# Kernel tuning notes

Hardware: AMD Instinct MI355X
Metric: run time of the kernel (lower is better)

Reference implementation:

```python
import jax, jax.numpy as jnp
import numpy as np

B, T, C = 2, 1024, 1024
HS = 64
H = C // HS                 # 16 wkv heads
C_ATT = 512
H_GQA = C_ATT // HS         # 8 kv heads
GROUP = H // H_GQA          # 2
D_DECAY, D_AAA, D_MV, D_GATE = 64, 64, 32, 160


def setup_inputs() -> dict:
    key = jax.random.key(0)
    ks = jax.random.split(key, 16)
    f32 = jnp.float32
    rn = lambda k, shp, s=0.02: jax.random.normal(k, shp, dtype=f32) * s
    return {
        'x': jax.random.normal(ks[0], (B, T, C), f32),
        'wkv_state_in': jnp.zeros((B, H, HS, HS), f32),
        'v_first_val': jax.random.normal(ks[1], (B, T, C), f32),
        'w0': jnp.linspace(-6.5, -1.5, C, dtype=f32).reshape(1, 1, C) + 0.5,
        'w1': rn(ks[2], (C, D_DECAY)), 'w2': rn(ks[3], (D_DECAY, C)),
        'a0': jnp.zeros((1, 1, C), f32),
        'a1': rn(ks[4], (C, D_AAA)), 'a2': rn(ks[5], (D_AAA, C)),
        'v0': jnp.ones((1, 1, C), f32),
        'v1': rn(ks[6], (C, D_MV)), 'v2': rn(ks[7], (D_MV, C)),
        'g1': rn(ks[8], (C, D_GATE)), 'g2': rn(ks[9], (D_GATE, C)),
        'k_k': jnp.full((1, 1, C), 0.85, f32),
        'k_a': jnp.ones((1, 1, C), f32),
        'r_k': rn(ks[10], (H, HS)),
        'Wq': rn(ks[11], (C, C)), 'Wk': rn(ks[12], (C_ATT, C)),
        'Wv': rn(ks[13], (C_ATT, C)), 'Wo': rn(ks[14], (C, C)),
        'ln_w': jnp.ones((C,), f32), 'ln_b': jnp.zeros((C,), f32),
    }


def _gqa_expand(t):
    # [B,T,C_ATT] -> repeat each kv head GROUP times -> [B,T,C]
    t = t.reshape(B, T, H_GQA, 1, HS)
    return jnp.broadcast_to(t, (B, T, H_GQA, GROUP, HS)).reshape(B, T, C)


def _wkv_scan(r, decay, k, v, a, b, S0):
    # all seq tensors [B,T,H,N]; scan over time with state S [B,H,N,N]
    seq = tuple(x.transpose(1, 0, 2, 3) for x in (r, decay, k, v, a, b))

    def step(S, ins):
        r_t, w_t, k_t, v_t, a_t, b_t = ins  # [B,H,N]
        sa = jnp.einsum('bhij,bhj->bhi', S, a_t)
        S = (S * w_t[:, :, None, :]
             + sa[..., None] * b_t[:, :, None, :]
             + v_t[..., None] * k_t[:, :, None, :])
        y = jnp.einsum('bhij,bhj->bhi', S, r_t)
        return S, y

    S_out, ys = jax.lax.scan(step, S0, seq)
    return ys.transpose(1, 0, 2, 3), S_out  # [B,T,H,N], [B,H,N,N]


def _forward(x, wkv_state_in, v_first_val, w0, w1, w2, a0, a1, a2, v0, v1, v2,
             g1, g2, k_k, k_a, r_k, Wq, Wk, Wv, Wo, ln_w, ln_b):
    r = x @ Wq.T                                   # [B,T,C]
    w = w0 + jnp.tanh(x @ w1) @ w2                 # decay logits [B,T,C]
    k = _gqa_expand(x @ Wk.T)                      # [B,T,C]
    v = _gqa_expand(x @ Wv.T)
    g = jax.nn.sigmoid(x @ g1) @ g2                # gate
    iclr = jax.nn.sigmoid(a0 + (x @ a1) @ a2)      # in-context learning rate

    kk = (k * k_k).reshape(B, T, H, HS)
    kk = kk / jnp.maximum(jnp.linalg.norm(kk, axis=-1, keepdims=True), 1e-12)
    kk = kk.reshape(B, T, C)

    iclr = 1.0 + (iclr - 1.0) * k_a
    k = k * iclr
    # layer_id > 0: mix v toward v_first
    v = v + (v_first_val - v) * jax.nn.sigmoid(v0 + (x @ v1) @ v2)

    decay = jnp.exp(-jnp.exp(w))                   # per-channel decay in (0,1)
    hv = lambda t: t.reshape(B, T, H, HS)
    xx, S_out = _wkv_scan(hv(r), hv(decay), hv(k), hv(v), hv(-kk), hv(kk * iclr), wkv_state_in)

    # GroupNorm with n_head groups, eps = 1e-5 * head_size
    mu = xx.mean(-1, keepdims=True)
    var = xx.var(-1, keepdims=True)
    xn = (xx - mu) * jax.lax.rsqrt(var + 1e-5 * HS)
    xn = xn.reshape(B, T, C) * ln_w + ln_b

    # r_k bonus term (standard RWKV7 epilogue)
    bonus = ((hv(r) * hv(k) * r_k).sum(-1, keepdims=True) * hv(v)).reshape(B, T, C)
    xn = xn + bonus

    out = (xn * g) @ Wo.T
    return out, S_out, v_first_val


def reference(x, wkv_state_in, v_first_val, w0, w1, w2, a0, a1, a2, v0, v1, v2,
              g1, g2, k_k, k_a, r_k, Wq, Wk, Wv, Wo, ln_w, ln_b):
    return _forward(x, wkv_state_in, v_first_val, w0, w1, w2, a0, a1, a2,
                    v0, v1, v2, g1, g2, k_k, k_a, r_k, Wq, Wk, Wv, Wo, ln_w, ln_b)
```

## Files before the change

### kernel.cpp

```cpp
#include <hip/hip_runtime.h>

typedef unsigned short u16;
typedef __attribute__((ext_vector_type(8))) short s16x8;
typedef __attribute__((ext_vector_type(4))) float f32x4;
typedef __attribute__((ext_vector_type(4))) int   i32x4;
typedef __attribute__((ext_vector_type(2))) int   i32x2;
typedef __attribute__((ext_vector_type(4))) unsigned short u16x4;

constexpr size_t OFF_XB   = 0;
constexpr size_t OFF_WQB  = OFF_XB   + 4194304;
constexpr size_t OFF_WKB  = OFF_WQB  + 2097152;
constexpr size_t OFF_WVB  = OFF_WKB  + 1048576;
constexpr size_t OFF_WOB  = OFF_WVB  + 1048576;
constexpr size_t OFF_W1T  = OFF_WOB  + 2097152;
constexpr size_t OFF_W2T  = OFF_W1T  + 786432;
constexpr size_t OFF_A2T  = OFF_W2T  + 131072;
constexpr size_t OFF_V2T  = OFF_A2T  + 131072;
constexpr size_t OFF_G2T  = OFF_V2T  + 65536;
constexpr size_t OFF_KQF  = OFF_G2T  + 327680;
constexpr size_t OFF_VQF  = OFF_KQF  + 4194304;
constexpr size_t OFF_URAW = OFF_VQF  + 4194304;
constexpr size_t OFF_UB   = OFF_URAW + 2621440;
constexpr size_t OFF_S2A  = OFF_UB   + 1572864;
constexpr size_t OFF_S2V  = OFF_S2A  + 8388608;
constexpr size_t OFF_GBUF = OFF_S2V  + 8388608;
constexpr size_t OFF_SEQ  = OFF_GBUF + 8388608;
constexpr size_t OFF_YBUF = OFF_SEQ  + 50331648;
constexpr size_t OFF_XGB  = OFF_YBUF + 8388608;

constexpr size_t OFF_VEPI = OFF_XB;
constexpr size_t OFF_DP   = OFF_W1T;

__device__ __forceinline__ u16 f2bf(float f){
  unsigned int u = __builtin_bit_cast(unsigned int, f);
  u = u + 0x7fffu + ((u >> 16) & 1u);
  return (u16)(u >> 16);
}
__device__ __forceinline__ int pk2(float a, float b){
  return (int)((unsigned)f2bf(a) | ((unsigned)f2bf(b) << 16));
}
__device__ __forceinline__ int cvtpk(float a, float b){
  int r;
  asm("v_cvt_pk_bf16_f32 %0, %1, %2" : "=v"(r) : "v"(a), "v"(b));
  return r;
}
__device__ __forceinline__ float bf2f(u16 h){
  return __builtin_bit_cast(float, ((unsigned)h) << 16);
}
__device__ __forceinline__ f32x4 cvt4(i32x2 v){
  unsigned a=(unsigned)v[0], b=(unsigned)v[1];
  f32x4 r;
  r[0]=__builtin_bit_cast(float, a<<16);
  r[1]=__builtin_bit_cast(float, a&0xffff0000u);
  r[2]=__builtin_bit_cast(float, b<<16);
  r[3]=__builtin_bit_cast(float, b&0xffff0000u);
  return r;
}

__device__ __forceinline__ void gload_lds16(const float* g, float* l){
  __builtin_amdgcn_global_load_lds((const __attribute__((address_space(1))) void*)g,
                                   (__attribute__((address_space(3))) void*)l, 16, 0, 0);
}
__device__ __forceinline__ void gload_lds16u(const u16* g, u16* l){
  __builtin_amdgcn_global_load_lds((const __attribute__((address_space(1))) void*)g,
                                   (__attribute__((address_space(3))) void*)l, 16, 0, 0);
}
__device__ __forceinline__ void gload_lds4(const float* g, float* l){
  __builtin_amdgcn_global_load_lds((const __attribute__((address_space(1))) void*)g,
                                   (__attribute__((address_space(3))) void*)l, 4, 0, 0);
}

constexpr size_t N_XB=2097152, N_WQ=1048576, N_WK=524288, N_WV=524288, N_WO=1048576,
  N_W1T=393216, N_W2T=65536, N_A2T=65536, N_V2T=32768, N_G2T=163840, N_VF=2097152;
constexpr size_t PREP_TOT = N_XB+N_WQ+N_WK+N_WV+N_WO+N_W1T+N_W2T+N_A2T+N_V2T+N_G2T+N_VF;

__global__ __launch_bounds__(256) void prep_kernel(char* ws, const float* x, const float* vfirst,
  const float* w1, const float* w2, const float* a1, const float* a2,
  const float* v1, const float* v2, const float* g1, const float* g2,
  const float* Wq, const float* Wk, const float* Wv, const float* Wo, float* dout)
{
  u16* XB=(u16*)(ws+OFF_XB); u16* WQB=(u16*)(ws+OFF_WQB); u16* WKB=(u16*)(ws+OFF_WKB);
  u16* WVB=(u16*)(ws+OFF_WVB); u16* WOB=(u16*)(ws+OFF_WOB); u16* W1T=(u16*)(ws+OFF_W1T);
  u16* W2T=(u16*)(ws+OFF_W2T); u16* A2T=(u16*)(ws+OFF_A2T); u16* V2T=(u16*)(ws+OFF_V2T);
  u16* G2T=(u16*)(ws+OFF_G2T);
  for (size_t idx=(size_t)blockIdx.x*256+threadIdx.x; idx<PREP_TOT; idx+=(size_t)gridDim.x*256){
    size_t r = idx;
    if (r < N_XB){ XB[r]=f2bf(x[r]); continue; } r-=N_XB;
    if (r < N_WQ){ WQB[r]=f2bf(Wq[r]); continue; } r-=N_WQ;
    if (r < N_WK){ WKB[r]=f2bf(Wk[r]); continue; } r-=N_WK;
    if (r < N_WV){ WVB[r]=f2bf(Wv[r]); continue; } r-=N_WV;
    if (r < N_WO){ WOB[r]=f2bf(Wo[r]); continue; } r-=N_WO;
    if (r < N_W1T){
      int n=(int)(r>>10), k=(int)(r&1023); float v=0.f;
      if (n<64) v=w1[(size_t)k*64+n];
      else if (n<128) v=a1[(size_t)k*64+(n-64)];
      else if (n<160) v=v1[(size_t)k*32+(n-128)];
      else if (n<320) v=g1[(size_t)k*160+(n-160)];
      W1T[r]=f2bf(v); continue; } r-=N_W1T;
    if (r < N_W2T){ int c=(int)(r>>6), d=(int)(r&63); W2T[r]=f2bf(w2[(size_t)d*1024+c]); continue; } r-=N_W2T;
    if (r < N_A2T){ int c=(int)(r>>6), d=(int)(r&63); A2T[r]=f2bf(a2[(size_t)d*1024+c]); continue; } r-=N_A2T;
    if (r < N_V2T){ int c=(int)(r>>5), d=(int)(r&31); V2T[r]=f2bf(v2[(size_t)d*1024+c]); continue; } r-=N_V2T;
    if (r < N_G2T){ int c=(int)(r/160), d=(int)(r%160); G2T[r]=f2bf(g2[(size_t)d*1024+c]); continue; } r-=N_G2T;
    dout[2228224 + r] = vfirst[r];
  }
}

__global__ __launch_bounds__(256) void gemm_kernel(int phase, char* ws,
  const float* w0b, const float* a0b, const float* v0b, float* dout)
{
  const u16* A; const u16* Bw;
  float* outF=nullptr; const float* bias=nullptr;
  char* SEQc=(char*)(ws+OFF_SEQ);
  u16* UBp=(u16*)(ws+OFF_UB);
  int lda=0, ldb=0, K=0, ldc=0, Nlim=1024, col0=0, outMode=0;
  int y = blockIdx.y;
  if (phase==0){
    A=(const u16*)(ws+OFF_XB); lda=1024; K=1024;
    if (y<8)      { Bw=(const u16*)(ws+OFF_WQB); ldb=1024; col0=y*128;       outMode=1; }
    else if (y<12){ Bw=(const u16*)(ws+OFF_WKB); ldb=1024; col0=(y-8)*128;   outF=(float*)(ws+OFF_KQF); ldc=512; Nlim=512; }
    else if (y<16){ Bw=(const u16*)(ws+OFF_WVB); ldb=1024; col0=(y-12)*128;  outF=(float*)(ws+OFF_VQF); ldc=512; Nlim=512; }
    else          { Bw=(const u16*)(ws+OFF_W1T); ldb=1024; col0=(y-16)*128;  outMode=4; Nlim=320; }
  } else if (phase==1){
    int seg=y>>3; col0=(y&7)*128;
    const int Ks[4]={64,64,32,160};
    const int Ao[4]={0,64,128,160};
    K=Ks[seg]; lda=384; ldb=K;
    A=(const u16*)(ws+OFF_UB) + Ao[seg];
    if (seg==0)     { Bw=(const u16*)(ws+OFF_W2T); outMode=2; bias=w0b; }
    else if (seg==1){ Bw=(const u16*)(ws+OFF_A2T); outMode=3; bias=a0b; outF=(float*)(ws+OFF_S2A); ldc=1024; }
    else if (seg==2){ Bw=(const u16*)(ws+OFF_V2T); outMode=3; bias=v0b; outF=(float*)(ws+OFF_S2V); ldc=1024; }
    else            { Bw=(const u16*)(ws+OFF_G2T); outF=(float*)(ws+OFF_GBUF); ldc=1024; }
  } else {
    A=(const u16*)(ws+OFF_XGB); lda=1024; K=1024;
    Bw=(const u16*)(ws+OFF_WOB); ldb=1024; col0=y*128; outF=dout; ldc=1024;
  }
  int m0 = blockIdx.x*128;
  __shared__ __align__(16) u16 As[2][4096];
  __shared__ __align__(16) u16 Bs[2][4096];
  int tid=threadIdx.x, l=tid&63, wv=tid>>6, wm=wv>>1, wn=wv&1;

  int srow = wv*32 + (l>>2);
  int cswz = (l&3) ^ ((srow>>1)&3);
  const u16* aP0 = A  + (size_t)(m0+srow)*lda      + cswz*8;
  const u16* aP1 = A  + (size_t)(m0+srow+16)*lda   + cswz*8;
  const u16* bP0 = Bw + (size_t)(col0+srow)*ldb    + cswz*8;
  const u16* bP1 = Bw + (size_t)(col0+srow+16)*ldb + cswz*8;

  f32x4 acc[4][4];
  #pragma unroll
  for (int i=0;i<4;i++)
    #pragma unroll
    for (int j=0;j<4;j++) acc[i][j]=(f32x4){0.f,0.f,0.f,0.f};

#define GSTAGE(b,k0) do{                                   \
    gload_lds16u(aP0 + (k0), &As[b][wv*1024]);             \
    gload_lds16u(aP1 + (k0), &As[b][wv*1024+512]);         \
    gload_lds16u(bP0 + (k0), &Bs[b][wv*1024]);             \
    gload_lds16u(bP1 + (k0), &Bs[b][wv*1024+512]);         \
  }while(0)

  GSTAGE(0,0);
  asm volatile("s_waitcnt vmcnt(0)" ::: "memory");
  __syncthreads();

  int rrow=l&15, ck=l>>4;
  for (int k0=0;k0<K;k0+=32){
    int cb=(k0>>5)&1;
    if (k0+32<K) GSTAGE(cb^1, k0+32);
    s16x8 af[4], bf[4];
    #pragma unroll
    for (int mt=0;mt<4;mt++){
      int ra = wm*64+mt*16+rrow;
      af[mt]=*(const s16x8*)(&As[cb][ra*32 + ((ck ^ ((ra>>1)&3))<<3)]);
    }
    #pragma unroll
    for (int nt=0;nt<4;nt++){
      int rb = wn*64+nt*16+rrow;
      bf[nt]=*(const s16x8*)(&Bs[cb][rb*32 + ((ck ^ ((rb>>1)&3))<<3)]);
    }
    #pragma unroll
    for (int mt=0;mt<4;mt++)
      #pragma unroll
      for (int nt=0;nt<4;nt++)
        acc[mt][nt]=__builtin_amdgcn_mfma_f32_16x16x32_bf16(af[mt],bf[nt],acc[mt][nt],0,0,0);
    __syncthreads();
  }
#undef GSTAGE
  #pragma unroll
  for (int mt=0;mt<4;mt++){
    #pragma unroll
    for (int nt=0;nt<4;nt++){
      int nglob = col0 + wn*64 + nt*16 + (l&15);
      if (nglob >= Nlim) continue;
      #pragma unroll
      for (int rg=0;rg<4;rg++){
        int mrow = m0 + wm*64 + mt*16 + ((l>>4)<<2) + rg;
        float val = acc[mt][nt][rg];
        if (outMode==0){
          outF[(size_t)mrow*ldc + nglob] = val;
        } else if (outMode==1){
          int b=mrow>>10, t=mrow&1023, h=nglob>>6, i=nglob&63;
          char* cbase = SEQc + (size_t)((b*16+h)*64 + (t>>4))*24576 + (size_t)(t&15)*896;
          *(u16*)(cbase + i*2) = f2bf(val);
        } else if (outMode==2){
          float w = bias[nglob] + val;
          float d = expf(-expf(w));
          int b=mrow>>10, t=mrow&1023, h=nglob>>6, i=nglob&63;
          char* cbase = SEQc + (size_t)((b*16+h)*64 + (t>>4))*24576 + (size_t)(t&15)*896;
          *(float*)(cbase + 640 + i*4) = d;
        } else if (outMode==3){
          float s = 1.0f/(1.0f+__expf(-(bias[nglob]+val)));
          outF[(size_t)mrow*ldc + nglob] = s;
        } else {
          float a = (nglob<64) ? tanhf(val)
                  : (nglob<160) ? val
                  : 1.0f/(1.0f+__expf(-val));
          UBp[(size_t)mrow*384 + nglob] = f2bf(a);
        }
      }
    }
  }
}

__global__ __launch_bounds__(256) void prep2_kernel(char* ws, const float* vfirst,
  const float* kk_s, const float* ka_s, const float* rkw)
{
  const float* KQF=(const float*)(ws+OFF_KQF);
  const float* VQF=(const float*)(ws+OFF_VQF);
  const float* ICLR=(const float*)(ws+OFF_S2A);
  const float* VMIX=(const float*)(ws+OFF_S2V);
  u16* VEPI=(u16*)(ws+OFF_VEPI);
  float* DPp=(float*)(ws+OFF_DP);
  int m=blockIdx.x, b=m>>10, t=m&1023;
  int tid=threadIdx.x, c0=tid*4, h=c0>>6, i0=c0&63, hk=h>>1;
  f32x4 kq=*(const f32x4*)(KQF+(size_t)m*512+hk*64+i0);
  f32x4 vq=*(const f32x4*)(VQF+(size_t)m*512+hk*64+i0);
  f32x4 ic=*(const f32x4*)(ICLR+(size_t)m*1024+c0);
  f32x4 vm=*(const f32x4*)(VMIX+(size_t)m*1024+c0);
  f32x4 vf=*(const f32x4*)(vfirst+(size_t)m*1024+c0);
  f32x4 kkc=*(const f32x4*)(kk_s+c0);
  f32x4 kac=*(const f32x4*)(ka_s+c0);
  f32x4 kk=kq*kkc;
  float ssq=kk[0]*kk[0]+kk[1]*kk[1]+kk[2]*kk[2]+kk[3]*kk[3];
  #pragma unroll
  for (int mk=1;mk<16;mk<<=1) ssq += __shfl_xor(ssq,mk);
  float scale = 1.0f / fmaxf(sqrtf(ssq), 1e-12f);
  int bh=b*16+h;
  char* cb = ws + OFF_SEQ + (size_t)(bh*64+(t>>4))*24576 + (size_t)(t&15)*896;
  u16x4 rv = *(const u16x4*)(cb + (size_t)i0*2);
  f32x4 rkv = *(const f32x4*)(rkw + h*64 + i0);
  f32x4 kf,vv,av,bv;
  float dpp=0.f;
  #pragma unroll
  for (int j=0;j<4;j++){
    float icc = 1.0f + (ic[j]-1.0f)*kac[j];
    float kkn = kk[j]*scale;
    kf[j]=kq[j]*icc;
    vv[j]=vq[j] + (vf[j]-vq[j])*vm[j];
    av[j]=-kkn;
    bv[j]=kkn*icc;
    dpp += bf2f(rv[j])*kf[j]*rkv[j];
  }
  #pragma unroll
  for (int mk=1;mk<16;mk<<=1) dpp += __shfl_xor(dpp,mk);
  if ((tid&15)==0) DPp[(size_t)bh*1024 + t] = dpp;
  i32x2 o;
  o[0]=pk2(kf[0],kf[1]); o[1]=pk2(kf[2],kf[3]);
  *(i32x2*)(cb + 128 + (size_t)i0*2) = o;
  o[0]=pk2(vv[0],vv[1]); o[1]=pk2(vv[2],vv[3]);
  *(i32x2*)(cb + 256 + (size_t)i0*2) = o;
  *(i32x2*)(VEPI + ((size_t)bh*1024+t)*64 + i0) = o;
  o[0]=pk2(av[0],av[1]); o[1]=pk2(av[2],av[3]);
  *(i32x2*)(cb + 384 + (size_t)i0*2) = o;
  o[0]=pk2(bv[0],bv[1]); o[1]=pk2(bv[2],bv[3]);
  *(i32x2*)(cb + 512 + (size_t)i0*2) = o;
}

#define MFMA32(a,b,c) __builtin_amdgcn_mfma_f32_16x16x32_bf16(a,b,c,0,0,0)

__global__ __launch_bounds__(64) void pre_kernel(char* ws){
  int bid=blockIdx.x;
  int l=threadIdx.x, c16=l&15, g=l>>4;
  char* chunk = ws + OFF_SEQ + (size_t)bid*24576;
  char* rec = chunk;

  __shared__ __align__(16) char SH[31776];
  u16* AT =(u16*)(SH+14336);
  u16* RT =(u16*)(SH+16640);
  u16* BT =(u16*)(SH+18944);
  u16* KT =(u16*)(SH+21248);
  u16* vbb=(u16*)(SH+23552);
  u16* BKL=(u16*)(SH+26656);
  float* WN  =(float*)(SH+0);
  u16* WY =(u16*)(SH+1088);
  u16* WB =(u16*)(SH+1888);
  u16* WK =(u16*)(SH+2688);
  u16* pbb=(u16*)(SH+3488);
  u16* zbb=(u16*)(SH+6592);
  float* rhsb=(float*)(SH+9696);
  float* gtmp=(float*)(SH+9696);
  const s16x8 zero8 = {0,0,0,0,0,0,0,0};
  const f32x4 zf4 = {0.f,0.f,0.f,0.f};

  #pragma unroll
  for (int q=0;q<14;q++)
    gload_lds16((const float*)(chunk + (size_t)q*1024) + l*4, (float*)(SH + q*1024));
  asm volatile("s_waitcnt vmcnt(0)" ::: "memory");
  __builtin_amdgcn_sched_barrier(0);

  float ptv[16]; float pp=1.f;
  #pragma unroll
  for (int t=0;t<16;t++){ pp *= *(const float*)(SH + t*896 + 640 + l*4); ptv[t]=pp; }
  float pL = ptv[15];
  *(float*)(rec + 10240 + (size_t)l*4) = pL;
  float rpL = __builtin_amdgcn_rcpf(pL);
  float bs[16], ks[16];
  u16 vcol[16];
  #pragma unroll
  for (int t=0;t<16;t++){
    float sc = pL * __builtin_amdgcn_rcpf(ptv[t]);
    bs[t] = bf2f(*(const u16*)(SH + t*896 + 512 + l*2)) * sc;
    ks[t] = bf2f(*(const u16*)(SH + t*896 + 128 + l*2)) * sc;
    vcol[t] = *(const u16*)(SH + t*896 + 256 + l*2);
  }
  {
    i32x4 o;
    o[0]=(int)((unsigned)vcol[0]|((unsigned)vcol[1]<<16));
    o[1]=(int)((unsigned)vcol[2]|((unsigned)vcol[3]<<16));
    o[2]=(int)((unsigned)vcol[4]|((unsigned)vcol[5]<<16));
    o[3]=(int)((unsigned)vcol[6]|((unsigned)vcol[7]<<16));
    *(i32x4*)(&vbb[l*24]) = o;
    o[0]=(int)((unsigned)vcol[8]|((unsigned)vcol[9]<<16));
    o[1]=(int)((unsigned)vcol[10]|((unsigned)vcol[11]<<16));
    o[2]=(int)((unsigned)vcol[12]|((unsigned)vcol[13]<<16));
    o[3]=(int)((unsigned)vcol[14]|((unsigned)vcol[15]<<16));
    *(i32x4*)(&vbb[l*24+8]) = o;
    o[0]=pk2(bs[0],bs[1]); o[1]=pk2(bs[2],bs[3]); o[2]=pk2(bs[4],bs[5]); o[3]=pk2(bs[6],bs[7]);
    *(i32x4*)(&BKL[l*40]) = o;
    o[0]=pk2(bs[8],bs[9]); o[1]=pk2(bs[10],bs[11]); o[2]=pk2(bs[12],bs[13]); o[3]=pk2(bs[14],bs[15]);
    *(i32x4*)(&BKL[l*40+8]) = o;
    o[0]=pk2(ks[0],ks[1]); o[1]=pk2(ks[2],ks[3]); o[2]=pk2(ks[4],ks[5]); o[3]=pk2(ks[6],ks[7]);
    *(i32x4*)(&BKL[l*40+16]) = o;
    o[0]=pk2(ks[8],ks[9]); o[1]=pk2(ks[10],ks[11]); o[2]=pk2(ks[12],ks[13]); o[3]=pk2(ks[14],ks[15]);
    *(i32x4*)(&BKL[l*40+24]) = o;
  }
  #pragma unroll
  for (int t=0;t<16;t++){
    float at = bf2f(*(const u16*)(SH + t*896 + 384 + l*2));
    float rt = bf2f(*(const u16*)(SH + t*896 +   0 + l*2));
    float pprev = (t==0) ? 1.f : ptv[t-1];
    AT[t*72+l] = f2bf(pprev*at);
    RT[t*72+l] = f2bf(ptv[t]*rt);
    BT[t*72+l] = f2bf(bs[t]*rpL);
    KT[t*72+l] = f2bf(ks[t]*rpL);
  }
  asm volatile("s_waitcnt lgkmcnt(0)" ::: "memory");
  __builtin_amdgcn_sched_barrier(0);

  {
    s16x8 afA[2], afR[2], bfB[2], bfK[2];
    #pragma unroll
    for (int Kt=0;Kt<2;Kt++){
      afA[Kt]=*(const s16x8*)(&AT[c16*72 + 32*Kt + 8*g]);
      afR[Kt]=*(const s16x8*)(&RT[c16*72 + 32*Kt + 8*g]);
      bfB[Kt]=*(const s16x8*)(&BT[c16*72 + 32*Kt + 8*g]);
      bfK[Kt]=*(const s16x8*)(&KT[c16*72 + 32*Kt + 8*g]);
    }
    f32x4 dNN=zf4, dNY=zf4, dBB=zf4, dBK=zf4;
    #pragma unroll
    for (int Kt=0;Kt<2;Kt++){
      dNN=MFMA32(afA[Kt],bfB[Kt],dNN);
      dNY=MFMA32(afA[Kt],bfK[Kt],dNY);
      dBB=MFMA32(afR[Kt],bfB[Kt],dBB);
      dBK=MFMA32(afR[Kt],bfK[Kt],dBK);
    }
    #pragma unroll
    for (int e=0;e<4;e++){
      int tR=4*g+e, sC=c16;
      WN[tR*17+sC] = dNN[e];
      WY[tR*24+sC] = (sC<tR)? f2bf(dNY[e]) : (u16)0;
      WB[tR*24+sC] = (sC<=tR)? f2bf(dBB[e]) : (u16)0;
      WK[tR*24+sC] = (sC<=tR)? f2bf(dBK[e]) : (u16)0;
    }
  }

  s16x8 vf[4];
  #pragma unroll
  for (int J=0;J<4;J++){
    vf[J]=zero8;
    if (g<2) vf[J]=*(const s16x8*)(&vbb[(16*J+c16)*24 + 8*g]);
  }
  {
    s16x8 wyf=zero8;
    if (g<2) wyf=*(const s16x8*)(&WY[c16*24 + 8*g]);
    f32x4 dR[4];
    #pragma unroll
    for (int J=0;J<4;J++){
      dR[J]=zf4;
      dR[J]=MFMA32(wyf,vf[J],dR[J]);
      #pragma unroll
      for (int e=0;e<4;e++)
        rhsb[(4*g+e)*68 + 16*J + c16] = dR[J][e];
    }
  }

  {
    float pv[16];
    #pragma unroll
    for (int t=0;t<16;t++) pv[t]=bf2f(AT[t*72+l]);
    #pragma unroll
    for (int t=1;t<16;t++)
      #pragma unroll
      for (int s=0;s<16;s++){
        if (s<t) pv[t] += WN[t*17+s]*pv[s];
      }
    i32x4 o;
    o[0]=pk2(pv[0],pv[1]); o[1]=pk2(pv[2],pv[3]); o[2]=pk2(pv[4],pv[5]); o[3]=pk2(pv[6],pv[7]);
    *(i32x4*)(&pbb[l*24]) = o;
    o[0]=pk2(pv[8],pv[9]); o[1]=pk2(pv[10],pv[11]); o[2]=pk2(pv[12],pv[13]); o[3]=pk2(pv[14],pv[15]);
    *(i32x4*)(&pbb[l*24+8]) = o;
  }

  {
    float zz[16];
    #pragma unroll
    for (int t=0;t<16;t++) zz[t]=rhsb[t*68+l];
    #pragma unroll
    for (int t=1;t<16;t++)
      #pragma unroll
      for (int s=0;s<16;s++){
        if (s<t) zz[t] += WN[t*17+s]*zz[s];
      }
    i32x4 o;
    o[0]=pk2(zz[0],zz[1]); o[1]=pk2(zz[2],zz[3]); o[2]=pk2(zz[4],zz[5]); o[3]=pk2(zz[6],zz[7]);
    *(i32x4*)(&zbb[l*24]) = o;
    o[0]=pk2(zz[8],zz[9]); o[1]=pk2(zz[10],zz[11]); o[2]=pk2(zz[12],zz[13]); o[3]=pk2(zz[14],zz[15]);
    *(i32x4*)(&zbb[l*24+8]) = o;
  }
  asm volatile("s_waitcnt lgkmcnt(0)" ::: "memory");
  __builtin_amdgcn_sched_barrier(0);

  {
    s16x8 wbf=zero8, wkf=zero8;
    if (g<2){
      wbf=*(const s16x8*)(&WB[c16*24 + 8*g]);
      wkf=*(const s16x8*)(&WK[c16*24 + 8*g]);
    }
    #pragma unroll
    for (int J=0;J<4;J++){
      s16x8 pfB=zero8, zfB=zero8;
      if (g<2){
        pfB=*(const s16x8*)(&pbb[(16*J+c16)*24 + 8*g]);
        zfB=*(const s16x8*)(&zbb[(16*J+c16)*24 + 8*g]);
      }
      f32x4 dG, dYl=zf4;
      #pragma unroll
      for (int e=0;e<4;e++) dG[e]=bf2f(RT[(4*g+e)*72 + 16*J + c16]);
      dG=MFMA32(wbf,pfB,dG);
      dYl=MFMA32(wbf,zfB,dYl);
      dYl=MFMA32(wkf,vf[J],dYl);
      #pragma unroll
      for (int e=0;e<4;e++) gtmp[(4*g+e)*68 + 16*J + c16]=dG[e];
      i32x2 o2; o2[0]=pk2(dYl[0],dYl[1]); o2[1]=pk2(dYl[2],dYl[3]);
      *(i32x2*)(rec + 10496 + (size_t)J*2560 + 2048 + (size_t)l*8) = o2;
    }
  }

  {
    s16x8 bk[4], pfr[4], bzv[4];
    #pragma unroll
    for (int nt=0;nt<4;nt++) bk[nt]=*(const s16x8*)(&BKL[(16*nt+c16)*40 + 8*g]);
    #pragma unroll
    for (int mt=0;mt<4;mt++)
      pfr[mt]= (g<2) ? *(const s16x8*)(&pbb[(16*mt+c16)*24 + 8*g]) : zero8;
    #pragma unroll
    for (int it=0;it<4;it++)
      bzv[it]= (g<2) ? *(const s16x8*)(&zbb[(16*it+c16)*24 + 8*g])
                     : *(const s16x8*)(&vbb[(16*it+c16)*24 + 8*(g-2)]);
    #pragma unroll
    for (int mt=0;mt<4;mt++){
      #pragma unroll
      for (int nt=0;nt<4;nt++){
        f32x4 dQ = MFMA32(pfr[mt], bk[nt], zf4);
        int kk = mt>>1, gq = ((mt&1)<<1) | (g>>1), jo = g&1;
        i32x2 o2; o2[0]=pk2(dQ[0],dQ[1]); o2[1]=pk2(dQ[2],dQ[3]);
        *(i32x2*)(rec + ((size_t)(kk*4+nt)*64 + (size_t)(c16 + 16*gq))*16 + 8*jo) = o2;
      }
    }
    #pragma unroll
    for (int jtp=0;jtp<4;jtp++){
      #pragma unroll
      for (int it=0;it<4;it++){
        f32x4 dc = MFMA32(bk[jtp], bzv[it], zf4);
        i32x2 o2; o2[0]=pk2(dc[0],dc[1]); o2[1]=pk2(dc[2],dc[3]);
        *(i32x2*)(rec + 10496 + (size_t)it*2560 + ((size_t)jtp*64 + l)*8) = o2;
      }
    }
  }

  #pragma unroll
  for (int kk=0;kk<2;kk++){
    f32x4 b0 = *(const f32x4*)(&gtmp[c16*68 + 32*kk + 8*g]);
    f32x4 b1 = *(const f32x4*)(&gtmp[c16*68 + 32*kk + 8*g + 4]);
    i32x4 o;
    o[0]=pk2(b0[0],b0[1]); o[1]=pk2(b0[2],b0[3]); o[2]=pk2(b1[0],b1[1]); o[3]=pk2(b1[2],b1[3]);
    *(i32x4*)(rec + 8192 + (size_t)(kk*64+l)*16) = o;
  }
}

__global__ __launch_bounds__(64) void scan2_kernel(char* ws, const float* S0, float* dout){
  float* YB=(float*)(ws+OFF_YBUF);
  const char* recb = ws + OFF_SEQ;
  int bid=blockIdx.x, bh=bid>>2, w=bid&3;
  int l=threadIdx.x, c16=l&15, g=l>>4;

  __shared__ __align__(16) char buf[3][13824];
  __shared__ __align__(16) u16 ST[16*88];

  f32x4 Sreg[4];
  #pragma unroll
  for (int jt=0;jt<4;jt++)
    Sreg[jt] = *(const f32x4*)(S0 + (size_t)bh*4096 + (size_t)(16*w+c16)*64 + 16*jt + 4*g);
  #pragma unroll
  for (int jt=0;jt<4;jt++){
    i32x2 p; p[0]=pk2(Sreg[jt][0],Sreg[jt][1]); p[1]=pk2(Sreg[jt][2],Sreg[jt][3]);
    *(i32x2*)(&ST[c16*88 + 16*jt + 4*g]) = p;
  }

  const char* rb = recb + (size_t)(bh*64)*24576;

  #pragma unroll
  for (int pc=0; pc<2; ++pc){
    const float* r = (const float*)(rb + (size_t)pc*24576);
    float* d = (float*)(&buf[pc][0]);
    #pragma unroll
    for (int q=0;q<10;q++) gload_lds16(r + q*256 + l*4, d + q*256);
    gload_lds4((const float*)(rb + (size_t)pc*24576 + 10240) + l, d + 2560);
    const float* rs = (const float*)(rb + (size_t)pc*24576 + 10496 + (size_t)w*2560);
    #pragma unroll
    for (int q=0;q<3;q++) gload_lds16(rs + q*256 + l*4, d + 2624 + q*256);
  }
  asm volatile("s_waitcnt vmcnt(14)" ::: "memory");
  __builtin_amdgcn_sched_barrier(0);

  float* yb0 = YB + (size_t)bh*65536;
  int cur=0;

  #pragma unroll 1
  for (int ch=0; ch<64; ++ch){
    asm volatile("s_waitcnt vmcnt(18)" ::: "memory");
    __builtin_amdgcn_sched_barrier(0);
    const char* bp = &buf[cur][0];

    s16x8 qf[4][2], gf[2], sB[2];
    #pragma unroll
    for (int kk=0;kk<2;kk++){
      #pragma unroll
      for (int jt=0;jt<4;jt++)
        qf[jt][kk]=*(const s16x8*)(bp + (size_t)((kk*4+jt)*64 + l)*16);
      gf[kk]=*(const s16x8*)(bp + 8192 + (size_t)(kk*64+l)*16);
      sB[kk]=*(const s16x8*)(&ST[c16*88 + 32*kk + 8*g]);
    }
    f32x4 pl4[4];
    #pragma unroll
    for (int jt=0;jt<4;jt++)
      pl4[jt]=*(const f32x4*)(bp + 10240 + (size_t)(16*jt+4*g)*4);
    i32x2 cfr[4];
    #pragma unroll
    for (int jt=0;jt<4;jt++)
      cfr[jt]=*(const i32x2*)(bp + 10496 + (size_t)(jt*64+l)*8);
    i32x2 ylv=*(const i32x2*)(bp + 12544 + (size_t)l*8);

    {
      int p2 = cur+2; if (p2>=3) p2-=3;
      int nc = ch+2; if (nc>63) nc=63;
      const float* r = (const float*)(rb + (size_t)nc*24576);
      float* d = (float*)(&buf[p2][0]);
      #pragma unroll
      for (int q=0;q<10;q++) gload_lds16(r + q*256 + l*4, d + q*256);
      gload_lds4((const float*)(rb + (size_t)nc*24576 + 10240) + l, d + 2560);
      const float* rs = (const float*)(rb + (size_t)nc*24576 + 10496 + (size_t)w*2560);
      #pragma unroll
      for (int q=0;q<3;q++) gload_lds16(rs + q*256 + l*4, d + 2624 + q*256);
    }
    __builtin_amdgcn_sched_barrier(0);

    f32x4 dy=cvt4(ylv);
    dy=MFMA32(gf[0],sB[0],dy); dy=MFMA32(gf[1],sB[1],dy);
    #pragma unroll
    for (int jt=0;jt<4;jt++){
      f32x4 acc = cvt4(cfr[jt]);
      acc = MFMA32(qf[jt][0], sB[0], acc);
      acc = MFMA32(qf[jt][1], sB[1], acc);
      #pragma unroll
      for (int e=0;e<4;e++) acc[e] = fmaf(pl4[jt][e], Sreg[jt][e], acc[e]);
      Sreg[jt]=acc;
    }
    #pragma unroll
    for (int jt=0;jt<4;jt++){
      i32x2 p; p[0]=cvtpk(Sreg[jt][0],Sreg[jt][1]); p[1]=cvtpk(Sreg[jt][2],Sreg[jt][3]);
      *(i32x2*)(&ST[c16*88 + 16*jt + 4*g]) = p;
    }
    {
      float* yb = yb0 + (size_t)ch*1024;
      #pragma unroll
      for (int e=0;e<4;e++)
        yb[(size_t)(4*g+e)*64 + 16*w + c16] = dy[e];
    }
    cur = (cur+1==3)?0:cur+1;
  }

  #pragma unroll
  for (int jt=0;jt<4;jt++)
    *(f32x4*)(dout + 2097152 + (size_t)bh*4096 + (size_t)(16*w+c16)*64 + 16*jt + 4*g) = Sreg[jt];
}

__global__ __launch_bounds__(256) void epi_kernel(char* ws, const float* lnw, const float* lnb)
{
  const float* YB=(const float*)(ws+OFF_YBUF);
  const u16* VEPI=(const u16*)(ws+OFF_VEPI);
  const float* DPp=(const float*)(ws+OFF_DP);
  const float* GB=(const float*)(ws+OFF_GBUF);
  u16* XGB=(u16*)(ws+OFF_XGB);
  int m=blockIdx.x, b=m>>10, t=m&1023;
  int tid=threadIdx.x, c0=tid*4, h=c0>>6, i0=c0&63;
  f32x4 y=*(const f32x4*)(YB + ((size_t)(b*16+h)*1024+t)*64 + i0);
  float s = y[0]+y[1]+y[2]+y[3];
  float ss= y[0]*y[0]+y[1]*y[1]+y[2]*y[2]+y[3]*y[3];
  #pragma unroll
  for (int mk=1;mk<16;mk<<=1){ s+=__shfl_xor(s,mk); ss+=__shfl_xor(ss,mk); }
  float mu=s*(1.0f/64.0f), var=ss*(1.0f/64.0f)-mu*mu;
  float inv=rsqrtf(var + 6.4e-4f);
  u16x4 v16=*(const u16x4*)(VEPI + ((size_t)(b*16+h)*1024+t)*64 + i0);
  float dp = DPp[(size_t)(b*16+h)*1024 + t];
  f32x4 gg=*(const f32x4*)(GB+(size_t)m*1024+c0);
  u16x4 outv;
  #pragma unroll
  for (int j=0;j<4;j++){
    float xn = (y[j]-mu)*inv*lnw[c0+j] + lnb[c0+j] + dp*bf2f(v16[j]);
    outv[j]=f2bf(xn*gg[j]);
  }
  *(u16x4*)(XGB+(size_t)m*1024+c0)=outv;
}

extern "C" void kernel_launch(void* const* d_in, const int* in_sizes, int n_in,
                              void* d_out, int out_size, void* d_ws, size_t ws_size,
                              hipStream_t stream) {
  const float* x      =(const float*)d_in[0];
  const float* S0     =(const float*)d_in[1];
  const float* vfirst =(const float*)d_in[2];
  const float* w0     =(const float*)d_in[3];
  const float* w1     =(const float*)d_in[4];
  const float* w2     =(const float*)d_in[5];
  const float* a0     =(const float*)d_in[6];
  const float* a1     =(const float*)d_in[7];
  const float* a2     =(const float*)d_in[8];
  const float* v0     =(const float*)d_in[9];
  const float* v1     =(const float*)d_in[10];
  const float* v2     =(const float*)d_in[11];
  const float* g1     =(const float*)d_in[12];
  const float* g2     =(const float*)d_in[13];
  const float* k_k    =(const float*)d_in[14];
  const float* k_a    =(const float*)d_in[15];
  const float* r_k    =(const float*)d_in[16];
  const float* Wq     =(const float*)d_in[17];
  const float* Wk     =(const float*)d_in[18];
  const float* Wv     =(const float*)d_in[19];
  const float* Wo     =(const float*)d_in[20];
  const float* ln_w   =(const float*)d_in[21];
  const float* ln_b   =(const float*)d_in[22];
  char* ws=(char*)d_ws;
  float* dout=(float*)d_out;

  prep_kernel<<<2048,256,0,stream>>>(ws,x,vfirst,w1,w2,a1,a2,v1,v2,g1,g2,Wq,Wk,Wv,Wo,dout);
  gemm_kernel<<<dim3(16,19),256,0,stream>>>(0,ws,w0,a0,v0,dout);
  gemm_kernel<<<dim3(16,32),256,0,stream>>>(1,ws,w0,a0,v0,dout);
  prep2_kernel<<<2048,256,0,stream>>>(ws,vfirst,k_k,k_a,r_k);
  pre_kernel<<<2048,64,0,stream>>>(ws);
  scan2_kernel<<<128,64,0,stream>>>(ws,S0,dout);
  epi_kernel<<<2048,256,0,stream>>>(ws,ln_w,ln_b);
  gemm_kernel<<<dim3(16,8),256,0,stream>>>(2,ws,w0,a0,v0,dout);
}
```

Before: 195.9 us.

## Replace LDS triple-buffered scan2 prefetch with register double-buffered direct global loads

The scan2 kernel no longer stages each chunk's records through a 3-deep LDS ring with async global-to-LDS loads and manual vmcnt waits. It now loads each chunk straight into one of two register sets (A/B) and alternates between them, issuing the load for chunk ch+2 right after the step on the current set. This removes the LDS round trip and the hand-placed waits, and frees about 41KB of LDS. In exchange it raises register pressure and leaves load latency hiding to the compiler's automatic waitcnt placement.

Result: no change. 195.4 us (-0.3%).

```diff
diff --git a/kernel.cpp b/kernel.cpp
--- a/kernel.cpp
+++ b/kernel.cpp
@@ -514,7 +514,6 @@
   int bid=blockIdx.x, bh=bid>>2, w=bid&3;
   int l=threadIdx.x, c16=l&15, g=l>>4;
 
-  __shared__ __align__(16) char buf[3][13824];
   __shared__ __align__(16) u16 ST[16*88];
 
   f32x4 Sreg[4];
@@ -528,87 +527,59 @@
   }
 
   const char* rb = recb + (size_t)(bh*64)*24576;
-
-  #pragma unroll
-  for (int pc=0; pc<2; ++pc){
-    const float* r = (const float*)(rb + (size_t)pc*24576);
-    float* d = (float*)(&buf[pc][0]);
-    #pragma unroll
-    for (int q=0;q<10;q++) gload_lds16(r + q*256 + l*4, d + q*256);
-    gload_lds4((const float*)(rb + (size_t)pc*24576 + 10240) + l, d + 2560);
-    const float* rs = (const float*)(rb + (size_t)pc*24576 + 10496 + (size_t)w*2560);
-    #pragma unroll
-    for (int q=0;q<3;q++) gload_lds16(rs + q*256 + l*4, d + 2624 + q*256);
-  }
-  asm volatile("s_waitcnt vmcnt(14)" ::: "memory");
-  __builtin_amdgcn_sched_barrier(0);
-
   float* yb0 = YB + (size_t)bh*65536;
-  int cur=0;
+
+#define DECLR(S) s16x8 qf##S[8]; s16x8 gf##S[2]; f32x4 pl##S[4]; i32x2 cf##S[4]; i32x2 yl##S;
+#define LOADR(S, nc) do{ \
+    const char* rp_ = rb + (size_t)(nc)*24576; \
+    _Pragma("unroll") \
+    for (int q_=0;q_<8;q_++) qf##S[q_] = *(const s16x8*)(rp_ + (size_t)q_*1024 + l*16); \
+    gf##S[0] = *(const s16x8*)(rp_ + 8192 + (size_t)l*16); \
+    gf##S[1] = *(const s16x8*)(rp_ + 9216 + (size_t)l*16); \
+    _Pragma("unroll") \
+    for (int jt_=0;jt_<4;jt_++) pl##S[jt_] = *(const f32x4*)(rp_ + 10240 + (size_t)(16*jt_+4*g)*4); \
+    _Pragma("unroll") \
+    for (int jt_=0;jt_<4;jt_++) cf##S[jt_] = *(const i32x2*)(rp_ + 10496 + (size_t)w*2560 + (size_t)(jt_*64+l)*8); \
+    yl##S = *(const i32x2*)(rp_ + 10496 + (size_t)w*2560 + 2048 + (size_t)l*8); \
+  }while(0)
+#define STEP(S, ch) do{ \
+    s16x8 sB0=*(const s16x8*)(&ST[c16*88 + 8*g]); \
+    s16x8 sB1=*(const s16x8*)(&ST[c16*88 + 32 + 8*g]); \
+    f32x4 dy=cvt4(yl##S); \
+    dy=MFMA32(gf##S[0],sB0,dy); dy=MFMA32(gf##S[1],sB1,dy); \
+    _Pragma("unroll") \
+    for (int jt_=0;jt_<4;jt_++){ \
+      f32x4 acc = cvt4(cf##S[jt_]); \
+      acc = MFMA32(qf##S[jt_], sB0, acc); \
+      acc = MFMA32(qf##S[4+jt_], sB1, acc); \
+      _Pragma("unroll") \
+      for (int e_=0;e_<4;e_++) acc[e_] = fmaf(pl##S[jt_][e_], Sreg[jt_][e_], acc[e_]); \
+      Sreg[jt_]=acc; \
+    } \
+    _Pragma("unroll") \
+    for (int jt_=0;jt_<4;jt_++){ \
+      i32x2 p_; p_[0]=cvtpk(Sreg[jt_][0],Sreg[jt_][1]); p_[1]=cvtpk(Sreg[jt_][2],Sreg[jt_][3]); \
+      *(i32x2*)(&ST[c16*88 + 16*jt_ + 4*g]) = p_; \
+    } \
+    { float* yb_ = yb0 + (size_t)(ch)*1024; \
+      _Pragma("unroll") \
+      for (int e_=0;e_<4;e_++) yb_[(size_t)(4*g+e_)*64 + 16*w + c16] = dy[e_]; } \
+  }while(0)
+
+  DECLR(A); DECLR(B);
+  LOADR(A, 0);
+  LOADR(B, 1);
 
   #pragma unroll 1
-  for (int ch=0; ch<64; ++ch){
-    asm volatile("s_waitcnt vmcnt(18)" ::: "memory");
-    __builtin_amdgcn_sched_barrier(0);
-    const char* bp = &buf[cur][0];
-
-    s16x8 qf[4][2], gf[2], sB[2];
-    #pragma unroll
-    for (int kk=0;kk<2;kk++){
-      #pragma unroll
-      for (int jt=0;jt<4;jt++)
-        qf[jt][kk]=*(const s16x8*)(bp + (size_t)((kk*4+jt)*64 + l)*16);
-      gf[kk]=*(const s16x8*)(bp + 8192 + (size_t)(kk*64+l)*16);
-      sB[kk]=*(const s16x8*)(&ST[c16*88 + 32*kk + 8*g]);
-    }
-    f32x4 pl4[4];
-    #pragma unroll
-    for (int jt=0;jt<4;jt++)
-      pl4[jt]=*(const f32x4*)(bp + 10240 + (size_t)(16*jt+4*g)*4);
-    i32x2 cfr[4];
-    #pragma unroll
-    for (int jt=0;jt<4;jt++)
-      cfr[jt]=*(const i32x2*)(bp + 10496 + (size_t)(jt*64+l)*8);
-    i32x2 ylv=*(const i32x2*)(bp + 12544 + (size_t)l*8);
-
-    {
-      int p2 = cur+2; if (p2>=3) p2-=3;
-      int nc = ch+2; if (nc>63) nc=63;
-      const float* r = (const float*)(rb + (size_t)nc*24576);
-      float* d = (float*)(&buf[p2][0]);
-      #pragma unroll
-      for (int q=0;q<10;q++) gload_lds16(r + q*256 + l*4, d + q*256);
-      gload_lds4((const float*)(rb + (size_t)nc*24576 + 10240) + l, d + 2560);
-      const float* rs = (const float*)(rb + (size_t)nc*24576 + 10496 + (size_t)w*2560);
-      #pragma unroll
-      for (int q=0;q<3;q++) gload_lds16(rs + q*256 + l*4, d + 2624 + q*256);
-    }
-    __builtin_amdgcn_sched_barrier(0);
-
-    f32x4 dy=cvt4(ylv);
-    dy=MFMA32(gf[0],sB[0],dy); dy=MFMA32(gf[1],sB[1],dy);
-    #pragma unroll
-    for (int jt=0;jt<4;jt++){
-      f32x4 acc = cvt4(cfr[jt]);
-      acc = MFMA32(qf[jt][0], sB[0], acc);
-      acc = MFMA32(qf[jt][1], sB[1], acc);
-      #pragma unroll
-      for (int e=0;e<4;e++) acc[e] = fmaf(pl4[jt][e], Sreg[jt][e], acc[e]);
-      Sreg[jt]=acc;
-    }
-    #pragma unroll
-    for (int jt=0;jt<4;jt++){
-      i32x2 p; p[0]=cvtpk(Sreg[jt][0],Sreg[jt][1]); p[1]=cvtpk(Sreg[jt][2],Sreg[jt][3]);
-      *(i32x2*)(&ST[c16*88 + 16*jt + 4*g]) = p;
-    }
-    {
-      float* yb = yb0 + (size_t)ch*1024;
-      #pragma unroll
-      for (int e=0;e<4;e++)
-        yb[(size_t)(4*g+e)*64 + 16*w + c16] = dy[e];
-    }
-    cur = (cur+1==3)?0:cur+1;
-  }
+  for (int ch=0; ch<64; ch+=2){
+    STEP(A, ch);
+    { int nc = ch+2; if (nc>63) nc=63; LOADR(A, nc); }
+    STEP(B, ch+1);
+    { int nc = ch+3; if (nc>63) nc=63; LOADR(B, nc); }
+  }
+#undef DECLR
+#undef LOADR
+#undef STEP
 
   #pragma unroll
   for (int jt=0;jt<4;jt++)
```
